# Kernel optimization log

Measured on AMD Instinct MI355X. Metric: run time of the kernel, lower is better.

The kernel has to match this reference:

```python
import jax, jax.numpy as jnp
import numpy as np

N_NODES = 100000
IN_F = 32
OUT_F = 32
EDGE_F = 16
N_EDGES = 400000
BN_EPS = 1e-5
LEAKY_SLOPE = 0.01


def setup_inputs() -> dict:
    key = jax.random.key(0)
    ks = jax.random.split(key, 8)
    node_feature = jax.random.normal(ks[0], (N_NODES, IN_F), dtype=jnp.float32)
    edge_feature = jax.random.normal(ks[1], (N_EDGES, EDGE_F), dtype=jnp.float32)
    nn_w = jax.random.normal(ks[2], (EDGE_F, IN_F * OUT_F), dtype=jnp.float32) * (1.0 / np.sqrt(EDGE_F))
    nn_b = jax.random.normal(ks[3], (IN_F * OUT_F,), dtype=jnp.float32) * 0.01
    root = jax.random.normal(ks[4], (IN_F, OUT_F), dtype=jnp.float32) * (1.0 / np.sqrt(IN_F))
    bias = jax.random.normal(ks[5], (OUT_F,), dtype=jnp.float32) * 0.01
    gamma = jnp.ones((OUT_F,), dtype=jnp.float32)
    beta = jnp.zeros((OUT_F,), dtype=jnp.float32)
    edge_index = jax.random.randint(ks[6], (2, N_EDGES), 0, N_NODES, dtype=jnp.int64)
    return {
        "node_feature": node_feature,
        "edge_feature": edge_feature,
        "nn_w": nn_w,
        "nn_b": nn_b,
        "root": root,
        "bias": bias,
        "gamma": gamma,
        "beta": beta,
        "edge_index": edge_index,
    }


def reference(node_feature, edge_feature, nn_w, nn_b, root, bias, gamma, beta, edge_index):
    src, dst = edge_index[0], edge_index[1]  # messages flow src -> dst (PyG source_to_target)
    # Edge MLP: per-edge weight matrix [E, IN_F, OUT_F]
    edge_w = (edge_feature @ nn_w + nn_b).reshape(-1, IN_F, OUT_F)
    # Gather source node features and apply per-edge matmul: [E, OUT_F]
    msg = jnp.einsum("ei,eio->eo", node_feature[src], edge_w)
    # Scatter-add aggregation at target nodes
    agg = jax.ops.segment_sum(msg, dst, num_segments=node_feature.shape[0])
    # Root transform + bias (NNConv root_weight=True, bias=True)
    h = agg + node_feature @ root + bias
    # BatchNorm1d (training mode: batch statistics over nodes, biased variance)
    mean = jnp.mean(h, axis=0)
    var = jnp.var(h, axis=0)
    h = (h - mean) * jax.lax.rsqrt(var + BN_EPS) * gamma + beta
    # LeakyReLU (default negative_slope = 0.01)
    return jnp.where(h >= 0, h, LEAKY_SLOPE * h)
```

## Files before the change

kernel.cpp:

```cpp
#include <hip/hip_runtime.h>

#define IN_F 32
#define OUT_F 32
#define EDGE_F 16
#define BN_EPS 1e-5f
#define SLOPE 0.01f

typedef _Float16 half_t;
typedef __attribute__((ext_vector_type(4))) _Float16 h4;
typedef __attribute__((ext_vector_type(8))) _Float16 f16x8;
typedef __attribute__((ext_vector_type(4))) float f32x4;

#define BCOLS 544
#define YSTRIDE 552

__global__ __launch_bounds__(256) void prep_bt_kernel(
    const float* __restrict__ W, const float* __restrict__ b,
    half_t* __restrict__ BtG, int* __restrict__ cnt32,
    float* __restrict__ stats, int NB) {
  int idx = blockIdx.x * 256 + threadIdx.x;
  if (idx < NB) cnt32[idx] = 0;
  if (idx < 64) stats[idx] = 0.f;
  if (idx >= BCOLS * 32) return;
  int o = idx & 31;
  int k = (idx >> 5) & 31;
  int fp = idx >> 10;
  float v;
  int col;
  if (fp < 16) { v = W[(size_t)fp * 1024 + k * 32 + o]; col = fp * 32 + o; }
  else         { v = b[k * 32 + o];                     col = 512 + o; }
  BtG[(size_t)col * 32 + k] = (half_t)v;
}

__global__ __launch_bounds__(256) void hist32_kernel(
    const int* __restrict__ ei, int* __restrict__ cnt, int E) {
  int e = blockIdx.x * 256 + threadIdx.x;
  if (e < E) atomicAdd(&cnt[ei[e] >> 5], 1);
}

__global__ __launch_bounds__(1024) void scan32_kernel(
    const int* __restrict__ cnt, int* __restrict__ rp,
    int* __restrict__ cursor, int NB, int E) {
  __shared__ int lds[1024];
  int t = threadIdx.x;
  int C = (NB + 1023) >> 10;
  int base = t * C;
  int s = 0;
  for (int c = 0; c < C; ++c) { int i = base + c; if (i < NB) s += cnt[i]; }
  lds[t] = s;
  __syncthreads();
  for (int off = 1; off < 1024; off <<= 1) {
    int u = (t >= off) ? lds[t - off] : 0;
    __syncthreads();
    lds[t] += u;
    __syncthreads();
  }
  int running = lds[t] - s;
  for (int c = 0; c < C; ++c) {
    int i = base + c;
    if (i < NB) { rp[i] = running; cursor[i] = running; running += cnt[i]; }
  }
  if (t == 0) rp[NB] = E;
}

__global__ __launch_bounds__(256) void scatter32_kernel(
    const int* __restrict__ ei, int* __restrict__ cursor,
    int* __restrict__ perm, int E) {
  int e = blockIdx.x * 256 + threadIdx.x;
  if (e < E) {
    int r = atomicAdd(&cursor[ei[e] >> 5], 1);
    perm[r] = e;
  }
}

__global__ __launch_bounds__(256, 4) void fused_kernel(
    const float* __restrict__ x, const half_t* __restrict__ BtG,
    const float* __restrict__ ef, const int* __restrict__ ei,
    const int* __restrict__ perm, const int* __restrict__ rp,
    float* __restrict__ out, int N, int E) {
  __shared__ half_t Yl[32][YSTRIDE];
  __shared__ float msgl[32][36];

  int b = blockIdx.x;
  int n0 = b * 32;
  int t = threadIdx.x;

  int wv = t >> 6, lane = t & 63, lr = lane & 15, kg = lane >> 4;
  int nh = wv & 1, ch = wv >> 1;
  int row = n0 + nh * 16 + lr;

  f16x8 a = (f16x8)(half_t)0.f;
  if (row < N) {
    float4 u0 = *(const float4*)(x + (size_t)row * 32 + kg * 8);
    float4 u1 = *(const float4*)(x + (size_t)row * 32 + kg * 8 + 4);
    a[0] = (half_t)u0.x; a[1] = (half_t)u0.y; a[2] = (half_t)u0.z; a[3] = (half_t)u0.w;
    a[4] = (half_t)u1.x; a[5] = (half_t)u1.y; a[6] = (half_t)u1.z; a[7] = (half_t)u1.w;
  }

  int nl0 = nh * 16 + kg * 4;
  for (int ci = 0; ci < 17; ++ci) {
    int col = (ch * 17 + ci) * 16 + lr;
    f16x8 bf = *(const f16x8*)(BtG + (size_t)col * 32 + kg * 8);
    f32x4 c = {0.f, 0.f, 0.f, 0.f};
    c = __builtin_amdgcn_mfma_f32_16x16x32_f16(a, bf, c, 0, 0, 0);
    Yl[nl0 + 0][col] = (half_t)c[0];
    Yl[nl0 + 1][col] = (half_t)c[1];
    Yl[nl0 + 2][col] = (half_t)c[2];
    Yl[nl0 + 3][col] = (half_t)c[3];
  }
  __syncthreads();

  int grp = t >> 3, oq = t & 7;
  int kb = rp[b], ke = rp[b + 1];
  for (int k = kb + grp; k < ke; k += 32) {
    int e = perm[k];
    int s = ei[e];
    int d = ei[E + e];
    int sl = s - n0;

    const float4* ep4 = (const float4*)(ef + (size_t)e * EDGE_F);
    float4 f0 = ep4[0], f1 = ep4[1], f2 = ep4[2], f3 = ep4[3];
    float efr[16] = {f0.x, f0.y, f0.z, f0.w, f1.x, f1.y, f1.z, f1.w,
                     f2.x, f2.y, f2.z, f2.w, f3.x, f3.y, f3.z, f3.w};

    float acc[4];
    {
      h4 xb = *(const h4*)(&Yl[sl][512 + oq * 4]);
      acc[0] = (float)xb[0]; acc[1] = (float)xb[1];
      acc[2] = (float)xb[2]; acc[3] = (float)xb[3];
    }
#pragma unroll
    for (int f = 0; f < 16; ++f) {
      h4 yv = *(const h4*)(&Yl[sl][f * 32 + oq * 4]);
      acc[0] = fmaf(efr[f], (float)yv[0], acc[0]);
      acc[1] = fmaf(efr[f], (float)yv[1], acc[1]);
      acc[2] = fmaf(efr[f], (float)yv[2], acc[2]);
      acc[3] = fmaf(efr[f], (float)yv[3], acc[3]);
    }

    msgl[grp][oq * 4 + 0] = acc[0];
    msgl[grp][oq * 4 + 1] = acc[1];
    msgl[grp][oq * 4 + 2] = acc[2];
    msgl[grp][oq * 4 + 3] = acc[3];
    asm volatile("s_waitcnt lgkmcnt(0)" ::: "memory");
    float* dp = out + (size_t)d * OUT_F;
    atomicAdd(dp + 0 * 8 + oq, msgl[grp][0 * 8 + oq]);
    atomicAdd(dp + 1 * 8 + oq, msgl[grp][1 * 8 + oq]);
    atomicAdd(dp + 2 * 8 + oq, msgl[grp][2 * 8 + oq]);
    atomicAdd(dp + 3 * 8 + oq, msgl[grp][3 * 8 + oq]);
  }
}

__global__ __launch_bounds__(256) void bn_stats_fused_kernel(
    const float* __restrict__ x, const float* __restrict__ root,
    const float* __restrict__ bias, float* __restrict__ h,
    float* __restrict__ stats, int N) {
  __shared__ float rl[1024];
  __shared__ float bl[32];
  __shared__ float ls[32], ls2[32];
  int t = threadIdx.x;
  for (int i = t; i < 1024; i += 256) rl[i] = root[i];
  if (t < 32) { bl[t] = bias[t]; ls[t] = 0.f; ls2[t] = 0.f; }
  __syncthreads();

  int o0 = (t & 7) * 4;
  float ts[4] = {0.f, 0.f, 0.f, 0.f};
  float tq[4] = {0.f, 0.f, 0.f, 0.f};
  int stride = gridDim.x * 256;
  for (int g = blockIdx.x * 256 + t; g < N * 8; g += stride) {
    int n = g >> 3;
    float4 a4 = *(const float4*)(h + (size_t)n * 32 + o0);
    float hv[4] = {bl[o0 + 0] + a4.x, bl[o0 + 1] + a4.y,
                   bl[o0 + 2] + a4.z, bl[o0 + 3] + a4.w};
    const float4* xr = (const float4*)(x + (size_t)n * 32);
#pragma unroll
    for (int q = 0; q < 8; ++q) {
      float4 xv = xr[q];
#pragma unroll
      for (int j = 0; j < 4; ++j) {
        hv[j] = fmaf(xv.x, rl[(q * 4 + 0) * 32 + o0 + j], hv[j]);
        hv[j] = fmaf(xv.y, rl[(q * 4 + 1) * 32 + o0 + j], hv[j]);
        hv[j] = fmaf(xv.z, rl[(q * 4 + 2) * 32 + o0 + j], hv[j]);
        hv[j] = fmaf(xv.w, rl[(q * 4 + 3) * 32 + o0 + j], hv[j]);
      }
    }
    *(float4*)(h + (size_t)n * 32 + o0) = make_float4(hv[0], hv[1], hv[2], hv[3]);
#pragma unroll
    for (int j = 0; j < 4; ++j) { ts[j] += hv[j]; tq[j] = fmaf(hv[j], hv[j], tq[j]); }
  }
#pragma unroll
  for (int j = 0; j < 4; ++j) {
    atomicAdd(&ls[o0 + j], ts[j]);
    atomicAdd(&ls2[o0 + j], tq[j]);
  }
  __syncthreads();
  if (t < 32) {
    atomicAdd(&stats[t], ls[t]);
    atomicAdd(&stats[32 + t], ls2[t]);
  }
}

__global__ __launch_bounds__(256) void bn_apply_kernel(
    float* __restrict__ h, const float* __restrict__ stats,
    const float* __restrict__ gamma, const float* __restrict__ beta,
    int total, float invN) {
  int t = blockIdx.x * blockDim.x + threadIdx.x;
  int i4 = t * 4;
  if (i4 >= total) return;
  float4 v = *(const float4*)(h + i4);
  float r[4] = {v.x, v.y, v.z, v.w};
  int o0 = i4 & 31;
#pragma unroll
  for (int j = 0; j < 4; ++j) {
    int o = o0 + j;
    float m = stats[o] * invN;
    float var = fmaf(-m, m, stats[32 + o] * invN);
    float sc = rsqrtf(var + BN_EPS) * gamma[o];
    float val = (r[j] - m) * sc + beta[o];
    r[j] = val >= 0.f ? val : SLOPE * val;
  }
  *(float4*)(h + i4) = make_float4(r[0], r[1], r[2], r[3]);
}

__global__ __launch_bounds__(256) void node_root_kernel(
    const float* __restrict__ x, const float* __restrict__ root,
    const float* __restrict__ bias, float* __restrict__ agg, int N) {
  __shared__ float rl[IN_F * OUT_F];
  __shared__ float bl[OUT_F];
  for (int t = threadIdx.x; t < IN_F * OUT_F; t += blockDim.x) rl[t] = root[t];
  if (threadIdx.x < OUT_F) bl[threadIdx.x] = bias[threadIdx.x];
  __syncthreads();
  int n = blockIdx.x * blockDim.x + threadIdx.x;
  bool valid = (n < N);
  int nu = valid ? n : 0;
  float xr[IN_F];
  const float4* xp = (const float4*)(x + (size_t)nu * IN_F);
#pragma unroll
  for (int q = 0; q < IN_F / 4; ++q) {
    float4 v = xp[q];
    xr[q * 4 + 0] = v.x; xr[q * 4 + 1] = v.y; xr[q * 4 + 2] = v.z; xr[q * 4 + 3] = v.w;
  }
  float acc[OUT_F];
#pragma unroll
  for (int o = 0; o < OUT_F; ++o) acc[o] = bl[o];
#pragma unroll
  for (int i = 0; i < IN_F; ++i) {
    float xi = xr[i];
#pragma unroll
    for (int o = 0; o < OUT_F; ++o) acc[o] = fmaf(xi, rl[i * OUT_F + o], acc[o]);
  }
  if (valid) {
    float4* op = (float4*)(agg + (size_t)n * OUT_F);
#pragma unroll
    for (int q = 0; q < OUT_F / 4; ++q)
      op[q] = make_float4(acc[q * 4 + 0], acc[q * 4 + 1], acc[q * 4 + 2], acc[q * 4 + 3]);
  }
}

__global__ __launch_bounds__(256) void edge_kernel(
    const float* __restrict__ x, const float* __restrict__ ef,
    const float* __restrict__ W, const float* __restrict__ b,
    const int* __restrict__ ei, float* __restrict__ agg, int E) {
  __shared__ float Wl[EDGE_F * IN_F * OUT_F];
  int e = blockIdx.x * blockDim.x + threadIdx.x;
  bool valid = (e < E);
  int eu = valid ? e : 0;
  int s = ei[eu];
  int d = ei[E + eu];
  float efr[EDGE_F];
  {
    const float4* ep = (const float4*)(ef + (size_t)eu * EDGE_F);
#pragma unroll
    for (int q = 0; q < EDGE_F / 4; ++q) {
      float4 v = ep[q];
      efr[q * 4 + 0] = v.x; efr[q * 4 + 1] = v.y;
      efr[q * 4 + 2] = v.z; efr[q * 4 + 3] = v.w;
    }
  }
  const float* xrow = x + (size_t)s * IN_F;
  float acc[OUT_F];
#pragma unroll
  for (int o = 0; o < OUT_F; ++o) acc[o] = 0.f;
  for (int t = threadIdx.x; t < IN_F * OUT_F; t += 256) Wl[t] = b[t];
  __syncthreads();
  for (int i = 0; i < IN_F; ++i) {
    float xi = xrow[i];
    const float* br = &Wl[i * OUT_F];
#pragma unroll
    for (int o = 0; o < OUT_F; ++o) acc[o] = fmaf(xi, br[o], acc[o]);
  }
  __syncthreads();
  for (int t = threadIdx.x; t < EDGE_F * IN_F * OUT_F / 4; t += 256)
    ((float4*)Wl)[t] = ((const float4*)W)[t];
  __syncthreads();
  for (int i = 0; i < IN_F; ++i) {
    float xi = xrow[i];
#pragma unroll
    for (int f = 0; f < EDGE_F; ++f) {
      float m = efr[f] * xi;
      const float* wr = &Wl[(f * IN_F + i) * OUT_F];
#pragma unroll
      for (int o = 0; o < OUT_F; ++o) acc[o] = fmaf(m, wr[o], acc[o]);
    }
  }
  if (valid) {
    float* dp = agg + (size_t)d * OUT_F;
#pragma unroll
    for (int o = 0; o < OUT_F; ++o) atomicAdd(dp + o, acc[o]);
  }
}

__global__ __launch_bounds__(256) void bn_stats_kernel(
    const float* __restrict__ h, float* __restrict__ stats, int total) {
  int t = blockIdx.x * blockDim.x + threadIdx.x;
  int stride = gridDim.x * blockDim.x;
  float s = 0.f, s2 = 0.f;
  for (int idx = t; idx < total; idx += stride) {
    float v = h[idx];
    s += v;
    s2 = fmaf(v, v, s2);
  }
  __shared__ float ls[256], ls2[256];
  ls[threadIdx.x] = s;
  ls2[threadIdx.x] = s2;
  __syncthreads();
  if (threadIdx.x < 32) {
    float a = ls[threadIdx.x], a2 = ls2[threadIdx.x];
    for (int j = 32 + threadIdx.x; j < 256; j += 32) { a += ls[j]; a2 += ls2[j]; }
    atomicAdd(&stats[threadIdx.x], a);
    atomicAdd(&stats[32 + threadIdx.x], a2);
  }
}

extern "C" void kernel_launch(void* const* d_in, const int* in_sizes, int n_in,
                              void* d_out, int out_size, void* d_ws, size_t ws_size,
                              hipStream_t stream) {
  const float* x     = (const float*)d_in[0];
  const float* ef    = (const float*)d_in[1];
  const float* W     = (const float*)d_in[2];
  const float* b     = (const float*)d_in[3];
  const float* root  = (const float*)d_in[4];
  const float* bias  = (const float*)d_in[5];
  const float* gamma = (const float*)d_in[6];
  const float* beta  = (const float*)d_in[7];
  const int*   ei    = (const int*)d_in[8];

  int N = in_sizes[0] / IN_F;
  int E = in_sizes[1] / EDGE_F;
  int total = N * OUT_F;
  int NB = (N + 31) / 32;

  float* out = (float*)d_out;
  char* wsb = (char*)d_ws;

  size_t off = 0;
  auto alloc = [&](size_t bytes) { size_t o = off; off = (off + bytes + 255) & ~(size_t)255; return o; };
  float*  stats  = (float*)(wsb + alloc(256));
  half_t* BtG    = (half_t*)(wsb + alloc((size_t)BCOLS * 32 * sizeof(half_t)));
  int*    cnt32  = (int*)(wsb + alloc((size_t)NB * 4));
  int*    rp32   = (int*)(wsb + alloc((size_t)(NB + 1) * 4));
  int*    cur32  = (int*)(wsb + alloc((size_t)NB * 4));
  int*    perm32 = (int*)(wsb + alloc((size_t)E * 4));
  size_t need = off;

  if (ws_size >= need) {
    int pgrid = (BCOLS * 32 + 255) / 256;
    int ngrid = (NB + 255) / 256;
    if (ngrid > pgrid) pgrid = ngrid;
    prep_bt_kernel<<<pgrid, 256, 0, stream>>>(W, b, BtG, cnt32, stats, NB);
    hist32_kernel<<<(E + 255) / 256, 256, 0, stream>>>(ei, cnt32, E);
    scan32_kernel<<<1, 1024, 0, stream>>>(cnt32, rp32, cur32, NB, E);
    scatter32_kernel<<<(E + 255) / 256, 256, 0, stream>>>(ei, cur32, perm32, E);
    hipMemsetAsync(out, 0, (size_t)total * sizeof(float), stream);
    fused_kernel<<<NB, 256, 0, stream>>>(x, BtG, ef, ei, perm32, rp32, out, N, E);
    bn_stats_fused_kernel<<<512, 256, 0, stream>>>(x, root, bias, out, stats, N);
  } else {
    hipMemsetAsync(stats, 0, 256, stream);
    node_root_kernel<<<(N + 255) / 256, 256, 0, stream>>>(x, root, bias, out, N);
    edge_kernel<<<(E + 255) / 256, 256, 0, stream>>>(x, ef, W, b, ei, out, E);
    bn_stats_kernel<<<1024, 256, 0, stream>>>(out, stats, total);
  }
  bn_apply_kernel<<<(total / 4 + 255) / 256, 256, 0, stream>>>(out, stats, gamma, beta, total, 1.0f / (float)N);
}
```

Baseline: 214.6 us.

## Replace global atomic scatter with dst-bucketed LDS aggregation via fp16 message buffer

Edges are now bucketed by both source block and destination block. The fused kernel writes fp16 per-edge messages to a workspace buffer in source-sorted order. A new aggregation kernel gathers those messages per destination block and accumulates them with LDS atomics, then writes the output once. This removes the output memset and the global float atomics. In exchange it adds a second histogram/scan/scatter, an extra kernel, roughly 25MB of message traffic, and fp16 rounding of messages.

```diff
diff --git a/kernel.cpp b/kernel.cpp
--- a/kernel.cpp
+++ b/kernel.cpp
@@ -16,10 +16,10 @@
 
 __global__ __launch_bounds__(256) void prep_bt_kernel(
     const float* __restrict__ W, const float* __restrict__ b,
-    half_t* __restrict__ BtG, int* __restrict__ cnt32,
+    half_t* __restrict__ BtG, int* __restrict__ cnt_s, int* __restrict__ cnt_d,
     float* __restrict__ stats, int NB) {
   int idx = blockIdx.x * 256 + threadIdx.x;
-  if (idx < NB) cnt32[idx] = 0;
+  if (idx < NB) { cnt_s[idx] = 0; cnt_d[idx] = 0; }
   if (idx < 64) stats[idx] = 0.f;
   if (idx >= BCOLS * 32) return;
   int o = idx & 31;
@@ -32,54 +32,66 @@
   BtG[(size_t)col * 32 + k] = (half_t)v;
 }
 
-__global__ __launch_bounds__(256) void hist32_kernel(
-    const int* __restrict__ ei, int* __restrict__ cnt, int E) {
+__global__ __launch_bounds__(256) void hist2_kernel(
+    const int* __restrict__ ei, int* __restrict__ cnt_s,
+    int* __restrict__ cnt_d, int E) {
   int e = blockIdx.x * 256 + threadIdx.x;
-  if (e < E) atomicAdd(&cnt[ei[e] >> 5], 1);
-}
-
-__global__ __launch_bounds__(1024) void scan32_kernel(
-    const int* __restrict__ cnt, int* __restrict__ rp,
-    int* __restrict__ cursor, int NB, int E) {
+  if (e < E) {
+    atomicAdd(&cnt_s[ei[e] >> 5], 1);
+    atomicAdd(&cnt_d[ei[E + e] >> 5], 1);
+  }
+}
+
+__global__ __launch_bounds__(1024) void scan2_kernel(
+    const int* __restrict__ cnt_s, int* __restrict__ rp_s, int* __restrict__ cur_s,
+    const int* __restrict__ cnt_d, int* __restrict__ rp_d, int* __restrict__ cur_d,
+    int NB, int E) {
   __shared__ int lds[1024];
   int t = threadIdx.x;
   int C = (NB + 1023) >> 10;
-  int base = t * C;
-  int s = 0;
-  for (int c = 0; c < C; ++c) { int i = base + c; if (i < NB) s += cnt[i]; }
-  lds[t] = s;
-  __syncthreads();
-  for (int off = 1; off < 1024; off <<= 1) {
-    int u = (t >= off) ? lds[t - off] : 0;
+  for (int pass = 0; pass < 2; ++pass) {
+    const int* cnt = pass ? cnt_d : cnt_s;
+    int* rp = pass ? rp_d : rp_s;
+    int* cur = pass ? cur_d : cur_s;
+    int base = t * C;
+    int s = 0;
+    for (int c = 0; c < C; ++c) { int i = base + c; if (i < NB) s += cnt[i]; }
+    lds[t] = s;
     __syncthreads();
-    lds[t] += u;
+    for (int off = 1; off < 1024; off <<= 1) {
+      int u = (t >= off) ? lds[t - off] : 0;
+      __syncthreads();
+      lds[t] += u;
+      __syncthreads();
+    }
+    int running = lds[t] - s;
+    for (int c = 0; c < C; ++c) {
+      int i = base + c;
+      if (i < NB) { rp[i] = running; cur[i] = running; running += cnt[i]; }
+    }
+    if (t == 0) rp[NB] = E;
     __syncthreads();
   }
-  int running = lds[t] - s;
-  for (int c = 0; c < C; ++c) {
-    int i = base + c;
-    if (i < NB) { rp[i] = running; cursor[i] = running; running += cnt[i]; }
-  }
-  if (t == 0) rp[NB] = E;
-}
-
-__global__ __launch_bounds__(256) void scatter32_kernel(
-    const int* __restrict__ ei, int* __restrict__ cursor,
-    int* __restrict__ perm, int E) {
+}
+
+__global__ __launch_bounds__(256) void scatter2_kernel(
+    const int* __restrict__ ei, int* __restrict__ cur_s, int* __restrict__ cur_d,
+    int* __restrict__ perm_s, int* __restrict__ perm_d, int E) {
   int e = blockIdx.x * 256 + threadIdx.x;
   if (e < E) {
-    int r = atomicAdd(&cursor[ei[e] >> 5], 1);
-    perm[r] = e;
-  }
-}
-
-__global__ __launch_bounds__(256, 4) void fused_kernel(
+    int s = ei[e], d = ei[E + e];
+    int rs = atomicAdd(&cur_s[s >> 5], 1);
+    perm_s[rs] = (e << 5) | (s & 31);
+    int rd = atomicAdd(&cur_d[d >> 5], 1);
+    perm_d[rd] = (rs << 5) | (d & 31);
+  }
+}
+
+__global__ __launch_bounds__(256, 4) void fused1_kernel(
     const float* __restrict__ x, const half_t* __restrict__ BtG,
-    const float* __restrict__ ef, const int* __restrict__ ei,
-    const int* __restrict__ perm, const int* __restrict__ rp,
-    float* __restrict__ out, int N, int E) {
+    const float* __restrict__ ef, const int* __restrict__ perm_s,
+    const int* __restrict__ rp_s, half_t* __restrict__ msg, int N) {
   __shared__ half_t Yl[32][YSTRIDE];
-  __shared__ float msgl[32][36];
 
   int b = blockIdx.x;
   int n0 = b * 32;
@@ -111,12 +123,10 @@
   __syncthreads();
 
   int grp = t >> 3, oq = t & 7;
-  int kb = rp[b], ke = rp[b + 1];
+  int kb = rp_s[b], ke = rp_s[b + 1];
   for (int k = kb + grp; k < ke; k += 32) {
-    int e = perm[k];
-    int s = ei[e];
-    int d = ei[E + e];
-    int sl = s - n0;
+    int pk = perm_s[k];
+    int e = pk >> 5, sl = pk & 31;
 
     const float4* ep4 = (const float4*)(ef + (size_t)e * EDGE_F);
     float4 f0 = ep4[0], f1 = ep4[1], f2 = ep4[2], f3 = ep4[3];
@@ -138,17 +148,41 @@
       acc[3] = fmaf(efr[f], (float)yv[3], acc[3]);
     }
 
-    msgl[grp][oq * 4 + 0] = acc[0];
-    msgl[grp][oq * 4 + 1] = acc[1];
-    msgl[grp][oq * 4 + 2] = acc[2];
-    msgl[grp][oq * 4 + 3] = acc[3];
-    asm volatile("s_waitcnt lgkmcnt(0)" ::: "memory");
-    float* dp = out + (size_t)d * OUT_F;
-    atomicAdd(dp + 0 * 8 + oq, msgl[grp][0 * 8 + oq]);
-    atomicAdd(dp + 1 * 8 + oq, msgl[grp][1 * 8 + oq]);
-    atomicAdd(dp + 2 * 8 + oq, msgl[grp][2 * 8 + oq]);
-    atomicAdd(dp + 3 * 8 + oq, msgl[grp][3 * 8 + oq]);
-  }
+    h4 hv;
+    hv[0] = (half_t)acc[0]; hv[1] = (half_t)acc[1];
+    hv[2] = (half_t)acc[2]; hv[3] = (half_t)acc[3];
+    *(h4*)(msg + (size_t)k * 32 + oq * 4) = hv;
+  }
+}
+
+__global__ __launch_bounds__(256) void agg2_kernel(
+    const half_t* __restrict__ msg, const int* __restrict__ perm_d,
+    const int* __restrict__ rp_d, float* __restrict__ out, int N) {
+  __shared__ float acc[32][32];
+  int b = blockIdx.x;
+  int n0 = b * 32;
+  int t = threadIdx.x;
+
+  ((float4*)&acc[0][0])[t] = make_float4(0.f, 0.f, 0.f, 0.f);
+  __syncthreads();
+
+  int grp = t >> 3, oq = t & 7;
+  int kb = rp_d[b], ke = rp_d[b + 1];
+  for (int k = kb + grp; k < ke; k += 32) {
+    int pk = perm_d[k];
+    int rs = pk >> 5, dl = pk & 31;
+    h4 v = *(const h4*)(msg + (size_t)rs * 32 + oq * 4);
+    atomicAdd(&acc[dl][oq * 4 + 0], (float)v[0]);
+    atomicAdd(&acc[dl][oq * 4 + 1], (float)v[1]);
+    atomicAdd(&acc[dl][oq * 4 + 2], (float)v[2]);
+    atomicAdd(&acc[dl][oq * 4 + 3], (float)v[3]);
+  }
+  __syncthreads();
+
+  int rowi = t >> 3, qq = t & 7;
+  int n = n0 + rowi;
+  if (n < N)
+    *(float4*)(out + (size_t)n * 32 + qq * 4) = *(float4*)&acc[rowi][qq * 4];
 }
 
 __global__ __launch_bounds__(256) void bn_stats_fused_kernel(
@@ -357,22 +391,29 @@
   auto alloc = [&](size_t bytes) { size_t o = off; off = (off + bytes + 255) & ~(size_t)255; return o; };
   float*  stats  = (float*)(wsb + alloc(256));
   half_t* BtG    = (half_t*)(wsb + alloc((size_t)BCOLS * 32 * sizeof(half_t)));
-  int*    cnt32  = (int*)(wsb + alloc((size_t)NB * 4));
-  int*    rp32   = (int*)(wsb + alloc((size_t)(NB + 1) * 4));
-  int*    cur32  = (int*)(wsb + alloc((size_t)NB * 4));
-  int*    perm32 = (int*)(wsb + alloc((size_t)E * 4));
+  int*    cnt_s  = (int*)(wsb + alloc((size_t)NB * 4));
+  int*    rp_s   = (int*)(wsb + alloc((size_t)(NB + 1) * 4));
+  int*    cur_s  = (int*)(wsb + alloc((size_t)NB * 4));
+  int*    cnt_d  = (int*)(wsb + alloc((size_t)NB * 4));
+  int*    rp_d   = (int*)(wsb + alloc((size_t)(NB + 1) * 4));
+  int*    cur_d  = (int*)(wsb + alloc((size_t)NB * 4));
+  int*    perm_s = (int*)(wsb + alloc((size_t)E * 4));
+  int*    perm_d = (int*)(wsb + alloc((size_t)E * 4));
+  half_t* msg    = (half_t*)(wsb + alloc((size_t)E * 32 * sizeof(half_t)));
   size_t need = off;
 
-  if (ws_size >= need) {
+  bool fits = ((size_t)E << 5) < 0x7FFFFFFF;
+
+  if (ws_size >= need && fits) {
     int pgrid = (BCOLS * 32 + 255) / 256;
     int ngrid = (NB + 255) / 256;
     if (ngrid > pgrid) pgrid = ngrid;
-    prep_bt_kernel<<<pgrid, 256, 0, stream>>>(W, b, BtG, cnt32, stats, NB);
-    hist32_kernel<<<(E + 255) / 256, 256, 0, stream>>>(ei, cnt32, E);
-    scan32_kernel<<<1, 1024, 0, stream>>>(cnt32, rp32, cur32, NB, E);
-    scatter32_kernel<<<(E + 255) / 256, 256, 0, stream>>>(ei, cur32, perm32, E);
-    hipMemsetAsync(out, 0, (size_t)total * sizeof(float), stream);
-    fused_kernel<<<NB, 256, 0, stream>>>(x, BtG, ef, ei, perm32, rp32, out, N, E);
+    prep_bt_kernel<<<pgrid, 256, 0, stream>>>(W, b, BtG, cnt_s, cnt_d, stats, NB);
+    hist2_kernel<<<(E + 255) / 256, 256, 0, stream>>>(ei, cnt_s, cnt_d, E);
+    scan2_kernel<<<1, 1024, 0, stream>>>(cnt_s, rp_s, cur_s, cnt_d, rp_d, cur_d, NB, E);
+    scatter2_kernel<<<(E + 255) / 256, 256, 0, stream>>>(ei, cur_s, cur_d, perm_s, perm_d, E);
+    fused1_kernel<<<NB, 256, 0, stream>>>(x, BtG, ef, perm_s, rp_s, msg, N);
+    agg2_kernel<<<NB, 256, 0, stream>>>(msg, perm_d, rp_d, out, N);
     bn_stats_fused_kernel<<<512, 256, 0, stream>>>(x, root, bias, out, stats, N);
   } else {
     hipMemsetAsync(stats, 0, 256, stream);
```

Result: slower. 298.1 us (+38.9%).
